# Performance work log

Measured on AMD Instinct MI355X. Metric: run time of the kernel, lower is better.

Reference implementation:

```python
import jax, jax.numpy as jnp
import numpy as np

BLOCK_SIZE = 64          # elements per quantization block
SCALER_BLOCK_SIZE = 256  # scalers per double-quantization block
OUT, IN = 11008, 4096
N_BLOCKS = OUT * IN // BLOCK_SIZE          # 704512
N_SCALER_BLOCKS = N_BLOCKS // SCALER_BLOCK_SIZE  # 2752

# QLoRA NF4 (4-bit NormalFloat) codebook
NF4_TABLE = np.array([
    -1.0, -0.6961928009986877, -0.5250730514526367, -0.39491748809814453,
    -0.28444138169288635, -0.18477343022823334, -0.10644006729125977,
    -0.029167551919817924, 0.0, 0.07958029955625534, 0.16093020141124725,
    0.24611230194568634, 0.33791524171829224, 0.44070982933044434,
    0.5626170039176941, 0.7229568362236023], dtype=np.float32)


def setup_inputs() -> dict:
    key = jax.random.key(0)
    k1, k2, k3, k4, k5 = jax.random.split(key, 5)
    x = jax.random.normal(k1, (4, 2048, IN), dtype=jnp.float32)
    # 4-bit codebook indices for each weight element
    qweight = jax.random.randint(k2, (OUT, IN), 0, 16, dtype=jnp.int32)
    # int8-style quantized per-block scalers (positive magnitudes)
    quantized_scalers = jax.random.randint(k3, (N_BLOCKS,), 1, 127, dtype=jnp.int32)
    # per scaler-block quantization factor (strictly positive, away from zero)
    quantization_factor = jax.random.uniform(k4, (N_SCALER_BLOCKS,), dtype=jnp.float32,
                                             minval=0.5, maxval=1.5) * 127.0
    scaler_mean = jax.random.uniform(k5, (1,), dtype=jnp.float32) * 0.01
    return {"x": x, "qweight": qweight, "quantized_scalers": quantized_scalers,
            "quantization_factor": quantization_factor, "scaler_mean": scaler_mean}


def dequantize_nf4(qweight, quantized_scalers, quantization_factor, scaler_mean, dtype):
    table = jnp.asarray(NF4_TABLE, dtype=dtype)
    # double-dequantize the per-block scalers
    scalers = (quantized_scalers.astype(dtype)
               / jnp.repeat(quantization_factor.astype(dtype), SCALER_BLOCK_SIZE)
               + scaler_mean.astype(dtype)[0])                      # [N_BLOCKS]
    # codebook lookup, then per-block scale
    w = table[qweight].reshape(N_BLOCKS, BLOCK_SIZE) * scalers[:, None]
    return w.reshape(OUT, IN)


def reference(x, qweight, quantized_scalers, quantization_factor, scaler_mean):
    # Faithful to LinearNF4.forward: F.linear(x, weight.to(x.dtype))
    w = dequantize_nf4(qweight, quantized_scalers, quantization_factor,
                       scaler_mean, x.dtype)                        # [OUT, IN]
    return jnp.einsum('bsi,oi->bso', x, w)
```

## Files before the change

### kernel.cpp

```cpp
#include <hip/hip_runtime.h>
#include <stdint.h>

#define M_ROWS 8192
#define K_DIM  4096
#define N_DIM  11008
#define KSTEPS (K_DIM / 64)

#define BM 256
#define BN 256
#define MBLKS (M_ROWS / BM)
#define NBLKS (N_DIM / BN)
#define NWG   (MBLKS * NBLKS)

typedef __attribute__((ext_vector_type(4))) float          f32x4;
typedef __attribute__((ext_vector_type(8))) __bf16         bf16x8;
typedef __attribute__((ext_vector_type(4))) int            i32x4;
typedef __attribute__((ext_vector_type(8))) unsigned short u16x8;

__constant__ float NF4_TBL[16] = {
    -1.0f, -0.6961928009986877f, -0.5250730514526367f, -0.39491748809814453f,
    -0.28444138169288635f, -0.18477343022823334f, -0.10644006729125977f,
    -0.029167551919817924f, 0.0f, 0.07958029955625534f, 0.16093020141124725f,
    0.24611230194568634f, 0.33791524171829224f, 0.44070982933044434f,
    0.5626170039176941f, 0.7229568362236023f};

__device__ __forceinline__ unsigned short f2bf(float f) {
  uint32_t u = __float_as_uint(f);
  u += 0x7fffu + ((u >> 16) & 1u);
  return (unsigned short)(u >> 16);
}

__device__ __forceinline__ void gload_lds16(const void* g, const void* l) {
  __builtin_amdgcn_global_load_lds(
      (const __attribute__((address_space(1))) void*)(uintptr_t)g,
      (__attribute__((address_space(3))) void*)(uint32_t)(uintptr_t)l,
      16, 0, 0);
}

__global__ void convert_x_kernel(const float* __restrict__ x,
                                 unsigned short* __restrict__ xb) {
  const long n8 = (long)M_ROWS * K_DIM / 8;
  for (long t = (long)blockIdx.x * blockDim.x + threadIdx.x; t < n8;
       t += (long)gridDim.x * blockDim.x) {
    const float* p = x + t * 8;
    f32x4 v0 = *(const f32x4*)p;
    f32x4 v1 = *(const f32x4*)(p + 4);
    u16x8 o;
    o[0] = f2bf(v0[0]); o[1] = f2bf(v0[1]); o[2] = f2bf(v0[2]); o[3] = f2bf(v0[3]);
    o[4] = f2bf(v1[0]); o[5] = f2bf(v1[1]); o[6] = f2bf(v1[2]); o[7] = f2bf(v1[3]);
    *(u16x8*)(xb + t * 8) = o;
  }
}

__global__ void dequant_w_kernel(const int* __restrict__ qw,
                                 const int* __restrict__ qs,
                                 const float* __restrict__ qf,
                                 const float* __restrict__ mean,
                                 unsigned short* __restrict__ wb) {
  __shared__ float tbl[16];
  if (threadIdx.x < 16) tbl[threadIdx.x] = NF4_TBL[threadIdx.x];
  __syncthreads();
  const float mu = mean[0];
  const long n8 = (long)N_DIM * K_DIM / 8;
  for (long t = (long)blockIdx.x * blockDim.x + threadIdx.x; t < n8;
       t += (long)gridDim.x * blockDim.x) {
    long f = t * 8;
    int  g = (int)(f >> 6);
    float s = (float)qs[g] / qf[g >> 8] + mu;
    i32x4 q0 = *(const i32x4*)(qw + f);
    i32x4 q1 = *(const i32x4*)(qw + f + 4);
    u16x8 o;
    o[0] = f2bf(tbl[q0[0]] * s); o[1] = f2bf(tbl[q0[1]] * s);
    o[2] = f2bf(tbl[q0[2]] * s); o[3] = f2bf(tbl[q0[3]] * s);
    o[4] = f2bf(tbl[q1[0]] * s); o[5] = f2bf(tbl[q1[1]] * s);
    o[6] = f2bf(tbl[q1[2]] * s); o[7] = f2bf(tbl[q1[3]] * s);
    *(u16x8*)(wb + f) = o;
  }
}

#define STG(GP, LB)                                                              \
  gload_lds16((GP) + (long)srow * K_DIM + scol, &LDSbuf[(LB) + wid * 1024]);     \
  gload_lds16((GP) + (long)(64 + srow) * K_DIM + scol,                           \
              &LDSbuf[(LB) + 8192 + wid * 1024]);

__global__ __launch_bounds__(512, 2) void gemm_8phase(
    const unsigned short* __restrict__ xb, const unsigned short* __restrict__ wb,
    float* __restrict__ C) {
  __align__(16) __shared__ unsigned char LDSbuf[131072];

  const int tid = threadIdx.x;
  const int wid = tid >> 6, lane = tid & 63;
  const int wr = wid >> 2, wc = wid & 3;
  const int r16 = lane & 15, hi = lane >> 4;

  const int wg = ((int)blockIdx.x & 7) * (NWG / 8) + ((int)blockIdx.x >> 3);
  const int mb = wg % MBLKS, nb = wg / MBLKS;
  const long m0g = (long)mb * BM, n0g = (long)nb * BN;

  const int srow = wid * 8 + (lane >> 3);
  const int scol = ((lane & 7) ^ (lane >> 3)) * 8;

  const int aoff = (wr * 128 + r16) * 128;
  const int boff = (wc * 64 + r16) * 128;
  const int kswz0 = ((hi ^ (r16 & 7)) << 4);
  const int kswz1 = kswz0 ^ 64;

  STG(xb + m0g * K_DIM,               0);
  STG(xb + (m0g + 128) * K_DIM,       16384);
  STG(wb + n0g * K_DIM,               65536);
  STG(wb + (n0g + 128) * K_DIM,       65536 + 16384);
  STG(xb + m0g * K_DIM + 64,          32768);
  STG(xb + (m0g + 128) * K_DIM + 64,  32768 + 16384);
  asm volatile("s_waitcnt vmcnt(4)");
  __builtin_amdgcn_sched_barrier(0);
  __builtin_amdgcn_s_barrier();

  bf16x8 af[8][2], bq[2][2];
  f32x4 acc[8][4] = {};

  for (int t = 0; t < KSTEPS; ++t) {
    const int cur = t & 1;
    const int cA = cur * 32768, cB = 65536 + cur * 32768;
    const int nB = 65536 + (cur ^ 1) * 32768;
    const long kB = (long)((t + 1 < KSTEPS ? t + 1 : KSTEPS - 1) * 64);
    const long kA = (long)((t + 2 < KSTEPS ? t + 2 : KSTEPS - 1) * 64);

#pragma unroll
    for (int m = 0; m < 4; ++m) {
      af[m][0] = *(const bf16x8*)&LDSbuf[cA + aoff + m * 2048 + kswz0];
      af[m][1] = *(const bf16x8*)&LDSbuf[cA + aoff + m * 2048 + kswz1];
    }
#pragma unroll
    for (int n = 0; n < 2; ++n) {
      bq[n][0] = *(const bf16x8*)&LDSbuf[cB + boff + n * 2048 + kswz0];
      bq[n][1] = *(const bf16x8*)&LDSbuf[cB + boff + n * 2048 + kswz1];
    }
    STG(wb + n0g * K_DIM + kB, nB);
    __builtin_amdgcn_s_barrier();
    __builtin_amdgcn_s_setprio(1);
#pragma unroll
    for (int m = 0; m < 4; ++m)
#pragma unroll
      for (int n = 0; n < 2; ++n) {
        acc[m][n] = __builtin_amdgcn_mfma_f32_16x16x32_bf16(af[m][0], bq[n][0], acc[m][n], 0, 0, 0);
        acc[m][n] = __builtin_amdgcn_mfma_f32_16x16x32_bf16(af[m][1], bq[n][1], acc[m][n], 0, 0, 0);
      }
    __builtin_amdgcn_s_setprio(0);
    __builtin_amdgcn_sched_barrier(0);
    __builtin_amdgcn_s_barrier();

#pragma unroll
    for (int m = 4; m < 8; ++m) {
      af[m][0] = *(const bf16x8*)&LDSbuf[cA + aoff + m * 2048 + kswz0];
      af[m][1] = *(const bf16x8*)&LDSbuf[cA + aoff + m * 2048 + kswz1];
    }
    STG(wb + (n0g + 128) * K_DIM + kB, nB + 16384);
    __builtin_amdgcn_s_barrier();
    __builtin_amdgcn_s_setprio(1);
#pragma unroll
    for (int m = 4; m < 8; ++m)
#pragma unroll
      for (int n = 0; n < 2; ++n) {
        acc[m][n] = __builtin_amdgcn_mfma_f32_16x16x32_bf16(af[m][0], bq[n][0], acc[m][n], 0, 0, 0);
        acc[m][n] = __builtin_amdgcn_mfma_f32_16x16x32_bf16(af[m][1], bq[n][1], acc[m][n], 0, 0, 0);
      }
    __builtin_amdgcn_s_setprio(0);
    __builtin_amdgcn_sched_barrier(0);
    __builtin_amdgcn_s_barrier();

#pragma unroll
    for (int n = 0; n < 2; ++n) {
      bq[n][0] = *(const bf16x8*)&LDSbuf[cB + boff + (2 + n) * 2048 + kswz0];
      bq[n][1] = *(const bf16x8*)&LDSbuf[cB + boff + (2 + n) * 2048 + kswz1];
    }
    STG(xb + m0g * K_DIM + kA, cA);
    __builtin_amdgcn_s_barrier();
    __builtin_amdgcn_s_setprio(1);
#pragma unroll
    for (int m = 0; m < 4; ++m)
#pragma unroll
      for (int n = 0; n < 2; ++n) {
        acc[m][2 + n] = __builtin_amdgcn_mfma_f32_16x16x32_bf16(af[m][0], bq[n][0], acc[m][2 + n], 0, 0, 0);
        acc[m][2 + n] = __builtin_amdgcn_mfma_f32_16x16x32_bf16(af[m][1], bq[n][1], acc[m][2 + n], 0, 0, 0);
      }
    __builtin_amdgcn_s_setprio(0);
    __builtin_amdgcn_sched_barrier(0);
    __builtin_amdgcn_s_barrier();

    STG(xb + (m0g + 128) * K_DIM + kA, cA + 16384);
    __builtin_amdgcn_s_barrier();
    __builtin_amdgcn_s_setprio(1);
#pragma unroll
    for (int m = 4; m < 8; ++m)
#pragma unroll
      for (int n = 0; n < 2; ++n) {
        acc[m][2 + n] = __builtin_amdgcn_mfma_f32_16x16x32_bf16(af[m][0], bq[n][0], acc[m][2 + n], 0, 0, 0);
        acc[m][2 + n] = __builtin_amdgcn_mfma_f32_16x16x32_bf16(af[m][1], bq[n][1], acc[m][2 + n], 0, 0, 0);
      }
    __builtin_amdgcn_s_setprio(0);
    asm volatile("s_waitcnt vmcnt(4)");
    __builtin_amdgcn_sched_barrier(0);
    __builtin_amdgcn_s_barrier();
    __builtin_amdgcn_sched_barrier(0);
  }

  const long crow = m0g + wr * 128 + hi * 4;
  const long ccol = n0g + wc * 64 + r16;
#pragma unroll
  for (int m = 0; m < 8; ++m)
#pragma unroll
    for (int n = 0; n < 4; ++n)
#pragma unroll
      for (int r = 0; r < 4; ++r)
        __builtin_nontemporal_store(
            acc[m][n][r], &C[(crow + m * 16 + r) * N_DIM + ccol + n * 16]);
}

__global__ __launch_bounds__(256) void gemm_fallback(
    const float* __restrict__ Xf, const int* __restrict__ qw,
    const int* __restrict__ qs, const float* __restrict__ qf,
    const float* __restrict__ meanp, float* __restrict__ C) {
  __shared__ unsigned short As[128 * 64];
  __shared__ unsigned short Bs[128 * 64];
  __shared__ float tbl[16];
  const int tid = threadIdx.x;
  if (tid < 16) tbl[tid] = NF4_TBL[tid];
  const float mu = meanp[0];
  const int nwg = (M_ROWS / 128) * (N_DIM / 128);
  const int wg = ((int)blockIdx.x & 7) * (nwg / 8) + ((int)blockIdx.x >> 3);
  const int mb = wg % (M_ROWS / 128), nb = wg / (M_ROWS / 128);
  const int m0 = mb * 128, n0 = nb * 128;
  const int wid = tid >> 6, lane = tid & 63;
  const int wr = wid >> 1, wcc = wid & 1;
  const int r16 = lane & 15, hi = lane >> 4;
  f32x4 acc[4][4] = {};
  for (int t = 0; t < KSTEPS; ++t) {
    const int k0 = t * 64;
    __syncthreads();
#pragma unroll
    for (int i = 0; i < 4; ++i) {
      int gi = i * 256 + tid;
      int row = gi >> 3, kq = (gi & 7) * 8;
      const float* px = Xf + (long)(m0 + row) * K_DIM + k0 + kq;
      f32x4 v0 = *(const f32x4*)px;
      f32x4 v1 = *(const f32x4*)(px + 4);
      u16x8 o;
      o[0] = f2bf(v0[0]); o[1] = f2bf(v0[1]); o[2] = f2bf(v0[2]); o[3] = f2bf(v0[3]);
      o[4] = f2bf(v1[0]); o[5] = f2bf(v1[1]); o[6] = f2bf(v1[2]); o[7] = f2bf(v1[3]);
      *(u16x8*)&As[row * 64 + kq] = o;
    }
#pragma unroll
    for (int i = 0; i < 4; ++i) {
      int gi = i * 256 + tid;
      int row = gi >> 3, kq = (gi & 7) * 8;
      const int* pq = qw + (long)(n0 + row) * K_DIM + k0 + kq;
      i32x4 q0 = *(const i32x4*)pq;
      i32x4 q1 = *(const i32x4*)(pq + 4);
      int g = (n0 + row) * (K_DIM / 64) + t;
      float s = (float)qs[g] / qf[g >> 8] + mu;
      u16x8 o;
      o[0] = f2bf(tbl[q0[0]] * s); o[1] = f2bf(tbl[q0[1]] * s);
      o[2] = f2bf(tbl[q0[2]] * s); o[3] = f2bf(tbl[q0[3]] * s);
      o[4] = f2bf(tbl[q1[0]] * s); o[5] = f2bf(tbl[q1[1]] * s);
      o[6] = f2bf(tbl[q1[2]] * s); o[7] = f2bf(tbl[q1[3]] * s);
      *(u16x8*)&Bs[row * 64 + kq] = o;
    }
    __syncthreads();
    bf16x8 afr[4][2], bfr[4][2];
#pragma unroll
    for (int i = 0; i < 4; ++i)
#pragma unroll
      for (int h = 0; h < 2; ++h) {
        afr[i][h] = *(const bf16x8*)&As[(wr * 64 + i * 16 + r16) * 64 + h * 32 + hi * 8];
        bfr[i][h] = *(const bf16x8*)&Bs[(wcc * 64 + i * 16 + r16) * 64 + h * 32 + hi * 8];
      }
#pragma unroll
    for (int i = 0; i < 4; ++i)
#pragma unroll
      for (int j = 0; j < 4; ++j) {
        acc[i][j] = __builtin_amdgcn_mfma_f32_16x16x32_bf16(afr[i][0], bfr[j][0], acc[i][j], 0, 0, 0);
        acc[i][j] = __builtin_amdgcn_mfma_f32_16x16x32_bf16(afr[i][1], bfr[j][1], acc[i][j], 0, 0, 0);
      }
  }
  const int crow = m0 + wr * 64 + hi * 4;
  const int ccol = n0 + wcc * 64 + r16;
#pragma unroll
  for (int i = 0; i < 4; ++i)
#pragma unroll
    for (int j = 0; j < 4; ++j)
#pragma unroll
      for (int r = 0; r < 4; ++r)
        C[(long)(crow + i * 16 + r) * N_DIM + (ccol + j * 16)] = acc[i][j][r];
}

extern "C" void kernel_launch(void* const* d_in, const int* in_sizes, int n_in,
                              void* d_out, int out_size, void* d_ws, size_t ws_size,
                              hipStream_t stream) {
  const float* x    = (const float*)d_in[0];
  const int*   qw   = (const int*)d_in[1];
  const int*   qs   = (const int*)d_in[2];
  const float* qf   = (const float*)d_in[3];
  const float* mean = (const float*)d_in[4];
  float* out = (float*)d_out;

  const size_t xb_bytes = (size_t)M_ROWS * K_DIM * 2;
  const size_t wb_bytes = (size_t)N_DIM * K_DIM * 2;

  if (ws_size >= xb_bytes + wb_bytes) {
    unsigned short* xb = (unsigned short*)d_ws;
    unsigned short* wb = (unsigned short*)((char*)d_ws + xb_bytes);
    convert_x_kernel<<<4096, 256, 0, stream>>>(x, xb);
    dequant_w_kernel<<<4096, 256, 0, stream>>>(qw, qs, qf, mean, wb);
    gemm_8phase<<<NWG, 512, 0, stream>>>(xb, wb, out);
  } else {
    gemm_fallback<<<(M_ROWS / 128) * (N_DIM / 128), 256, 0, stream>>>(
        x, qw, qs, qf, mean, out);
  }
}
```

Measured before the change: 798.0 us.

## Triple-buffer A tiles and remove intra-iteration barriers in GEMM main loop

Replaces the 8-phase GEMM loop with a pipeline that keeps three LDS buffers for the activation tile, growing LDS from 128KB to 160KB. A prefetch now writes into a buffer that no wave reads during the current step, so the per-phase workgroup barriers are removed and only one barrier per K step remains. A fragments are now read two 16-row blocks at a time into alternating register sets, interleaved with finer MFMA clusters, which reduces register pressure and should keep the matrix units busier. The risks are LDS pressure at the hardware limit and relying on the compiler schedule now that fewer barriers separate phases. An unused CLUSTER macro is added and fallback-kernel variables are renamed.

Result: faster. 777.2 us (-2.6%).

```diff
diff --git a/kernel.cpp b/kernel.cpp
--- a/kernel.cpp
+++ b/kernel.cpp
@@ -83,10 +83,34 @@
   gload_lds16((GP) + (long)(64 + srow) * K_DIM + scol,                           \
               &LDSbuf[(LB) + 8192 + wid * 1024]);
 
-__global__ __launch_bounds__(512, 2) void gemm_8phase(
+#define SB __builtin_amdgcn_sched_barrier(0)
+
+#define RD_A2(DST, MB, SA)                                                        \
+  DST[0][0] = *(const bf16x8*)&LDSbuf[(SA) + aoff + (MB) * 2048 + kswz0];         \
+  DST[0][1] = *(const bf16x8*)&LDSbuf[(SA) + aoff + (MB) * 2048 + kswz1];         \
+  DST[1][0] = *(const bf16x8*)&LDSbuf[(SA) + aoff + ((MB) + 1) * 2048 + kswz0];   \
+  DST[1][1] = *(const bf16x8*)&LDSbuf[(SA) + aoff + ((MB) + 1) * 2048 + kswz1];
+
+#define RD_B2(NB, CB)                                                             \
+  bq[NB][0]     = *(const bf16x8*)&LDSbuf[(CB) + boff + (NB) * 2048 + kswz0];     \
+  bq[NB][1]     = *(const bf16x8*)&LDSbuf[(CB) + boff + (NB) * 2048 + kswz1];     \
+  bq[NB + 1][0] = *(const bf16x8*)&LDSbuf[(CB) + boff + ((NB) + 1) * 2048 + kswz0];\
+  bq[NB + 1][1] = *(const bf16x8*)&LDSbuf[(CB) + boff + ((NB) + 1) * 2048 + kswz1];
+
+#define MFP(MI, AF, AI, NI)                                                       \
+  acc[MI][NI] = __builtin_amdgcn_mfma_f32_16x16x32_bf16(AF[AI][0], bq[NI][0], acc[MI][NI], 0, 0, 0); \
+  acc[MI][NI] = __builtin_amdgcn_mfma_f32_16x16x32_bf16(AF[AI][1], bq[NI][1], acc[MI][NI], 0, 0, 0);
+
+#define CLUSTER(MB, AF, N0)                                                       \
+  __builtin_amdgcn_s_setprio(1);                                                  \
+  MFP(MB, AF, 0, N0) MFP(MB, AF, 1, N0)                                           \
+  MFP((MB) + 1 - 1 + 1, AF, 1, (N0) + 1)                           \
+  __builtin_amdgcn_s_setprio(0);
+
+__global__ __launch_bounds__(512, 2) void gemm_pipe(
     const unsigned short* __restrict__ xb, const unsigned short* __restrict__ wb,
     float* __restrict__ C) {
-  __align__(16) __shared__ unsigned char LDSbuf[131072];
+  __align__(16) __shared__ unsigned char LDSbuf[163840];
 
   const int tid = threadIdx.x;
   const int wid = tid >> 6, lane = tid & 63;
@@ -105,103 +129,76 @@
   const int kswz0 = ((hi ^ (r16 & 7)) << 4);
   const int kswz1 = kswz0 ^ 64;
 
-  STG(xb + m0g * K_DIM,               0);
-  STG(xb + (m0g + 128) * K_DIM,       16384);
-  STG(wb + n0g * K_DIM,               65536);
-  STG(wb + (n0g + 128) * K_DIM,       65536 + 16384);
-  STG(xb + m0g * K_DIM + 64,          32768);
-  STG(xb + (m0g + 128) * K_DIM + 64,  32768 + 16384);
+  STG(xb + m0g * K_DIM,              0);
+  STG(xb + (m0g + 128) * K_DIM,      16384);
+  STG(wb + n0g * K_DIM,              98304);
+  STG(wb + (n0g + 128) * K_DIM,      98304 + 16384);
+  STG(xb + m0g * K_DIM + 64,         32768);
+  STG(xb + (m0g + 128) * K_DIM + 64, 32768 + 16384);
   asm volatile("s_waitcnt vmcnt(4)");
   __builtin_amdgcn_sched_barrier(0);
   __builtin_amdgcn_s_barrier();
 
-  bf16x8 af[8][2], bq[2][2];
+  bf16x8 af_a[2][2], af_b[2][2], bq[4][2];
   f32x4 acc[8][4] = {};
+
+  int sAr = 0, sAn = 32768, sAs = 65536;
 
   for (int t = 0; t < KSTEPS; ++t) {
     const int cur = t & 1;
-    const int cA = cur * 32768, cB = 65536 + cur * 32768;
-    const int nB = 65536 + (cur ^ 1) * 32768;
+    const int cB = 98304 + cur * 32768;
+    const int nB = 98304 + (cur ^ 1) * 32768;
     const long kB = (long)((t + 1 < KSTEPS ? t + 1 : KSTEPS - 1) * 64);
     const long kA = (long)((t + 2 < KSTEPS ? t + 2 : KSTEPS - 1) * 64);
 
-#pragma unroll
-    for (int m = 0; m < 4; ++m) {
-      af[m][0] = *(const bf16x8*)&LDSbuf[cA + aoff + m * 2048 + kswz0];
-      af[m][1] = *(const bf16x8*)&LDSbuf[cA + aoff + m * 2048 + kswz1];
-    }
-#pragma unroll
-    for (int n = 0; n < 2; ++n) {
-      bq[n][0] = *(const bf16x8*)&LDSbuf[cB + boff + n * 2048 + kswz0];
-      bq[n][1] = *(const bf16x8*)&LDSbuf[cB + boff + n * 2048 + kswz1];
-    }
+    RD_A2(af_a, 0, sAr);
+    RD_B2(0, cB);
+    SB;
+    RD_B2(2, cB);
     STG(wb + n0g * K_DIM + kB, nB);
-    __builtin_amdgcn_s_barrier();
-    __builtin_amdgcn_s_setprio(1);
-#pragma unroll
-    for (int m = 0; m < 4; ++m)
-#pragma unroll
-      for (int n = 0; n < 2; ++n) {
-        acc[m][n] = __builtin_amdgcn_mfma_f32_16x16x32_bf16(af[m][0], bq[n][0], acc[m][n], 0, 0, 0);
-        acc[m][n] = __builtin_amdgcn_mfma_f32_16x16x32_bf16(af[m][1], bq[n][1], acc[m][n], 0, 0, 0);
-      }
-    __builtin_amdgcn_s_setprio(0);
-    __builtin_amdgcn_sched_barrier(0);
-    __builtin_amdgcn_s_barrier();
-
-#pragma unroll
-    for (int m = 4; m < 8; ++m) {
-      af[m][0] = *(const bf16x8*)&LDSbuf[cA + aoff + m * 2048 + kswz0];
-      af[m][1] = *(const bf16x8*)&LDSbuf[cA + aoff + m * 2048 + kswz1];
-    }
+    __builtin_amdgcn_s_setprio(1);
+    MFP(0, af_a, 0, 0) MFP(1, af_a, 1, 0) MFP(0, af_a, 0, 1) MFP(1, af_a, 1, 1)
+    __builtin_amdgcn_s_setprio(0);
+    SB;
+    RD_A2(af_b, 2, sAr);
     STG(wb + (n0g + 128) * K_DIM + kB, nB + 16384);
-    __builtin_amdgcn_s_barrier();
-    __builtin_amdgcn_s_setprio(1);
-#pragma unroll
-    for (int m = 4; m < 8; ++m)
-#pragma unroll
-      for (int n = 0; n < 2; ++n) {
-        acc[m][n] = __builtin_amdgcn_mfma_f32_16x16x32_bf16(af[m][0], bq[n][0], acc[m][n], 0, 0, 0);
-        acc[m][n] = __builtin_amdgcn_mfma_f32_16x16x32_bf16(af[m][1], bq[n][1], acc[m][n], 0, 0, 0);
-      }
-    __builtin_amdgcn_s_setprio(0);
-    __builtin_amdgcn_sched_barrier(0);
-    __builtin_amdgcn_s_barrier();
-
-#pragma unroll
-    for (int n = 0; n < 2; ++n) {
-      bq[n][0] = *(const bf16x8*)&LDSbuf[cB + boff + (2 + n) * 2048 + kswz0];
-      bq[n][1] = *(const bf16x8*)&LDSbuf[cB + boff + (2 + n) * 2048 + kswz1];
-    }
-    STG(xb + m0g * K_DIM + kA, cA);
-    __builtin_amdgcn_s_barrier();
-    __builtin_amdgcn_s_setprio(1);
-#pragma unroll
-    for (int m = 0; m < 4; ++m)
-#pragma unroll
-      for (int n = 0; n < 2; ++n) {
-        acc[m][2 + n] = __builtin_amdgcn_mfma_f32_16x16x32_bf16(af[m][0], bq[n][0], acc[m][2 + n], 0, 0, 0);
-        acc[m][2 + n] = __builtin_amdgcn_mfma_f32_16x16x32_bf16(af[m][1], bq[n][1], acc[m][2 + n], 0, 0, 0);
-      }
-    __builtin_amdgcn_s_setprio(0);
-    __builtin_amdgcn_sched_barrier(0);
-    __builtin_amdgcn_s_barrier();
-
-    STG(xb + (m0g + 128) * K_DIM + kA, cA + 16384);
-    __builtin_amdgcn_s_barrier();
-    __builtin_amdgcn_s_setprio(1);
-#pragma unroll
-    for (int m = 4; m < 8; ++m)
-#pragma unroll
-      for (int n = 0; n < 2; ++n) {
-        acc[m][2 + n] = __builtin_amdgcn_mfma_f32_16x16x32_bf16(af[m][0], bq[n][0], acc[m][2 + n], 0, 0, 0);
-        acc[m][2 + n] = __builtin_amdgcn_mfma_f32_16x16x32_bf16(af[m][1], bq[n][1], acc[m][2 + n], 0, 0, 0);
-      }
+    __builtin_amdgcn_s_setprio(1);
+    MFP(0, af_a, 0, 2) MFP(1, af_a, 1, 2) MFP(0, af_a, 0, 3) MFP(1, af_a, 1, 3)
+    __builtin_amdgcn_s_setprio(0);
+    SB;
+    STG(xb + m0g * K_DIM + kA, sAs);
+    __builtin_amdgcn_s_setprio(1);
+    MFP(2, af_b, 0, 2) MFP(3, af_b, 1, 2) MFP(2, af_b, 0, 3) MFP(3, af_b, 1, 3)
+    __builtin_amdgcn_s_setprio(0);
+    SB;
+    RD_A2(af_a, 4, sAr);
+    STG(xb + (m0g + 128) * K_DIM + kA, sAs + 16384);
+    __builtin_amdgcn_s_setprio(1);
+    MFP(2, af_b, 0, 0) MFP(3, af_b, 1, 0) MFP(2, af_b, 0, 1) MFP(3, af_b, 1, 1)
+    __builtin_amdgcn_s_setprio(0);
+    SB;
+    __builtin_amdgcn_s_setprio(1);
+    MFP(4, af_a, 0, 0) MFP(5, af_a, 1, 0) MFP(4, af_a, 0, 1) MFP(5, af_a, 1, 1)
+    __builtin_amdgcn_s_setprio(0);
+    SB;
+    RD_A2(af_b, 6, sAr);
+    __builtin_amdgcn_s_setprio(1);
+    MFP(4, af_a, 0, 2) MFP(5, af_a, 1, 2) MFP(4, af_a, 0, 3) MFP(5, af_a, 1, 3)
+    __builtin_amdgcn_s_setprio(0);
+    SB;
+    __builtin_amdgcn_s_setprio(1);
+    MFP(6, af_b, 0, 2) MFP(7, af_b, 1, 2) MFP(6, af_b, 0, 3) MFP(7, af_b, 1, 3)
+    __builtin_amdgcn_s_setprio(0);
+    SB;
+    __builtin_amdgcn_s_setprio(1);
+    MFP(6, af_b, 0, 0) MFP(7, af_b, 1, 0) MFP(6, af_b, 0, 1) MFP(7, af_b, 1, 1)
     __builtin_amdgcn_s_setprio(0);
     asm volatile("s_waitcnt vmcnt(4)");
     __builtin_amdgcn_sched_barrier(0);
     __builtin_amdgcn_s_barrier();
     __builtin_amdgcn_sched_barrier(0);
+
+    int tmp = sAr; sAr = sAn; sAn = sAs; sAs = tmp;
   }
 
   const long crow = m0g + wr * 128 + hi * 4;
@@ -228,10 +225,10 @@
   const float mu = meanp[0];
   const int nwg = (M_ROWS / 128) * (N_DIM / 128);
   const int wg = ((int)blockIdx.x & 7) * (nwg / 8) + ((int)blockIdx.x >> 3);
-  const int mb = wg % (M_ROWS / 128), nb = wg / (M_ROWS / 128);
-  const int m0 = mb * 128, n0 = nb * 128;
+  const int mbf = wg % (M_ROWS / 128), nbf = wg / (M_ROWS / 128);
+  const int m0 = mbf * 128, n0 = nbf * 128;
   const int wid = tid >> 6, lane = tid & 63;
-  const int wr = wid >> 1, wcc = wid & 1;
+  const int wrf = wid >> 1, wcc = wid & 1;
   const int r16 = lane & 15, hi = lane >> 4;
   f32x4 acc[4][4] = {};
   for (int t = 0; t < KSTEPS; ++t) {
@@ -271,7 +268,7 @@
     for (int i = 0; i < 4; ++i)
 #pragma unroll
       for (int h = 0; h < 2; ++h) {
-        afr[i][h] = *(const bf16x8*)&As[(wr * 64 + i * 16 + r16) * 64 + h * 32 + hi * 8];
+        afr[i][h] = *(const bf16x8*)&As[(wrf * 64 + i * 16 + r16) * 64 + h * 32 + hi * 8];
         bfr[i][h] = *(const bf16x8*)&Bs[(wcc * 64 + i * 16 + r16) * 64 + h * 32 + hi * 8];
       }
 #pragma unroll
@@ -282,7 +279,7 @@
         acc[i][j] = __builtin_amdgcn_mfma_f32_16x16x32_bf16(afr[i][1], bfr[j][1], acc[i][j], 0, 0, 0);
       }
   }
-  const int crow = m0 + wr * 64 + hi * 4;
+  const int crow = m0 + wrf * 64 + hi * 4;
   const int ccol = n0 + wcc * 64 + r16;
 #pragma unroll
   for (int i = 0; i < 4; ++i)
@@ -311,7 +308,7 @@
     unsigned short* wb = (unsigned short*)((char*)d_ws + xb_bytes);
     convert_x_kernel<<<4096, 256, 0, stream>>>(x, xb);
     dequant_w_kernel<<<4096, 256, 0, stream>>>(qw, qs, qf, mean, wb);
-    gemm_8phase<<<NWG, 512, 0, stream>>>(xb, wb, out);
+    gemm_pipe<<<NWG, 512, 0, stream>>>(xb, wb, out);
   } else {
     gemm_fallback<<<(M_ROWS / 128) * (N_DIM / 128), 256, 0, stream>>>(
         x, qw, qs, qf, mean, out);
```
